# Performance work log

Measured on AMD Instinct MI355X. Metric: run time of the kernel, lower is better.

## Reference

```python
import jax, jax.numpy as jnp
import numpy as np
import math

BLOCK = 4      # block_size
N_HEADS = 8
DIM = 512
COND = 512
B = 2
HWU = 32       # h = w = u
NN = 7         # 'cross' neighbors


def _layernorm(x, w, eps=1e-5):
    mu = x.mean(-1, keepdims=True)
    var = ((x - mu) ** 2).mean(-1, keepdims=True)
    return (x - mu) * jax.lax.rsqrt(var + eps) * w


def _modulate(x, shift, scale):
    return x * (1.0 + scale) + shift


def _rotate_half(x):
    x1, x2 = jnp.split(x, 2, axis=-1)
    return jnp.concatenate([-x2, x1], axis=-1)


def _rot(x, cos, sin):
    return x * cos + _rotate_half(x) * sin


def setup_inputs() -> dict:
    key = jax.random.key(0)
    ks = jax.random.split(key, 16)
    h = w = u = HWU
    S = h * w * u
    dh = DIM // N_HEADS
    P = BLOCK ** 3
    ib = HWU // BLOCK                       # blocks per axis = 8
    nb = ib ** 3                            # 512 blocks per batch

    x = jax.random.normal(ks[0], (B, S, DIM), jnp.float32)
    c = jax.random.normal(ks[1], (B, COND), jnp.float32)

    # proper rotary tables over P block-local positions
    inv = 1.0 / (10000.0 ** (np.arange(0, dh, 2, dtype=np.float32) / dh))
    f = np.arange(P, dtype=np.float32)[:, None] * inv[None, :]
    emb = np.concatenate([f, f], axis=-1)          # [P, dh]
    cos = jnp.asarray(np.cos(emb))[None, :, None, :]
    sin = jnp.asarray(np.sin(emb))[None, :, None, :]

    # neighbor indices (cross pattern) on the block grid, mirroring get_neighbor_indices
    grid = np.stack(np.meshgrid(np.arange(B), np.arange(ib), np.arange(ib), np.arange(ib), indexing='ij'), axis=-1)
    shifts = np.array([[0, 0, 0, 0], [0, 0, -1, 0], [0, -1, 0, 0], [0, 0, 0, -1],
                       [0, 0, 1, 0], [0, 1, 0, 0], [0, 0, 0, 1]])
    nbr = grid[..., None, :] + shifts[None, None, None, None, :, :]
    nbr[..., 1:] = np.clip(nbr[..., 1:], 0, ib - 1)
    flat = (nbr[..., 0] * ib * ib * ib + nbr[..., 1] * ib * ib
            + nbr[..., 2] * ib + nbr[..., 3]).reshape(B * nb, NN)
    # every other block is 'nonzero' -> Nsel = 512
    nonzero_blocks = np.arange(0, B * nb, 2, dtype=np.int64)
    nonzero_blocks_neighbor = flat[nonzero_blocks].reshape(-1).astype(np.int64)

    s = 0.02
    params = dict(
        norm1_w=jnp.ones((DIM,), jnp.float32),
        qkv_w=s * jax.random.normal(ks[2], (3 * DIM, DIM), jnp.float32),
        out_w=s * jax.random.normal(ks[3], (DIM, DIM), jnp.float32),
        norm2_w=jnp.ones((DIM,), jnp.float32),
        mlp_w1=s * jax.random.normal(ks[4], (4 * DIM, DIM), jnp.float32),
        mlp_b1=jnp.zeros((4 * DIM,), jnp.float32),
        mlp_w2=s * jax.random.normal(ks[5], (DIM, 4 * DIM), jnp.float32),
        mlp_b2=jnp.zeros((DIM,), jnp.float32),
        adaln_w=s * jax.random.normal(ks[6], (6 * DIM, COND), jnp.float32),
        adaln_b=jnp.zeros((6 * DIM,), jnp.float32),
        kv_empty=s * jax.random.normal(ks[7], (1, P, 2 * DIM), jnp.float32),
    )
    return dict(x=x, c=c, cos_q=cos, sin_q=sin, cos_k=cos, sin_k=sin,
                nonzero_blocks=jnp.asarray(nonzero_blocks),
                nonzero_blocks_neighbor=jnp.asarray(nonzero_blocks_neighbor),
                h=h, w=w, u=u, **params)


def reference(x, c, cos_q, sin_q, cos_k, sin_k, nonzero_blocks, nonzero_blocks_neighbor,
              h, w, u, norm1_w, qkv_w, out_w, norm2_w, mlp_w1, mlp_b1, mlp_w2, mlp_b2,
              adaln_w, adaln_b, kv_empty):
    Bx, S, D = x.shape
    bs = BLOCK
    ix, iy, iz = h // bs, w // bs, u // bs
    nb = ix * iy * iz
    P = bs ** 3
    dh = D // N_HEADS
    Nsel = nonzero_blocks.shape[0]

    def transform(t):
        t = t.reshape(Bx, ix, bs, iy, bs, iz, bs, D)
        return t.transpose(0, 1, 3, 5, 2, 4, 6, 7).reshape(Bx, nb, P, D)

    def inverse_transform(t):
        t = t.reshape(Bx, ix, iy, iz, bs, bs, bs, D)
        return t.transpose(0, 1, 4, 2, 5, 3, 6, 7).reshape(Bx, S, D)

    mods = (c @ adaln_w.T + adaln_b)[:, None, :]         # [B,1,6D]
    shift_msa, scale_msa, gate_msa, shift_mlp, scale_mlp, gate_mlp = jnp.split(mods, 6, axis=-1)

    x_skip = x
    xm = _modulate(_layernorm(x, norm1_w), shift_msa, scale_msa)
    xb = transform(xm).reshape(Bx * nb, P, D)
    x_sel = xb[nonzero_blocks]                            # [Nsel,P,D]

    qkv = x_sel @ qkv_w.T                                 # [Nsel,P,3D]
    q, k, v = jnp.split(qkv, 3, axis=-1)
    k_e, v_e = jnp.split(kv_empty, 2, axis=-1)            # [1,P,D]
    k_full = jnp.broadcast_to(k_e, (Bx * nb, P, D)).at[nonzero_blocks].set(k)
    v_full = jnp.broadcast_to(v_e, (Bx * nb, P, D)).at[nonzero_blocks].set(v)
    kn = k_full[nonzero_blocks_neighbor]                  # [Nsel*NN,P,D]
    vn = v_full[nonzero_blocks_neighbor]

    qh = _rot(q.reshape(Nsel, P, N_HEADS, dh), cos_q, sin_q)
    kh = _rot(kn.reshape(Nsel * NN, P, N_HEADS, dh), cos_k, sin_k)
    kh = kh.reshape(Nsel, NN * P, N_HEADS, dh)
    vh = vn.reshape(Nsel, NN * P, N_HEADS, dh)

    scores = jnp.einsum('bqhd,bkhd->bhqk', qh, kh) / math.sqrt(dh)
    attn = jax.nn.softmax(scores, axis=-1)
    out = jnp.einsum('bhqk,bkhd->bqhd', attn, vh).reshape(Nsel, P, D)

    xz = jnp.zeros((Bx * nb, P, D), out.dtype).at[nonzero_blocks].set(out)
    x_attn = inverse_transform(xz.reshape(Bx, nb, P, D))
    x1 = x_skip + gate_msa * (x_attn @ out_w.T)

    x2 = _modulate(_layernorm(x1, norm2_w), shift_mlp, scale_mlp)
    mlp = jax.nn.gelu(x2 @ mlp_w1.T + mlp_b1, approximate=True) @ mlp_w2.T + mlp_b2
    return x1 + gate_mlp * mlp
```

## Files before the change

kernel.cpp:

```cpp
#include <hip/hip_runtime.h>
#include <cstdint>
#include <cstddef>

typedef unsigned short u16;
typedef __attribute__((ext_vector_type(8))) __bf16 bf16x8;
typedef __attribute__((ext_vector_type(4))) float f32x4;

typedef __attribute__((address_space(1))) const void GAS;
typedef __attribute__((address_space(3))) void LAS;

__device__ __forceinline__ void gld_lds16(const void* g, void* l) {
  __builtin_amdgcn_global_load_lds((GAS*)g, (LAS*)l, 16, 0, 0);
}

__device__ __forceinline__ u16 f2bf(float f) {
  union { float f; unsigned u; } x; x.f = f;
  unsigned r = x.u + 0x7FFFu + ((x.u >> 16) & 1u);
  return (u16)(r >> 16);
}
__device__ __forceinline__ float bf2f(u16 s) {
  union { unsigned u; float f; } x; x.u = ((unsigned)s) << 16;
  return x.f;
}
__device__ __forceinline__ f32x4 mfma16(bf16x8 a, bf16x8 b, f32x4 c) {
  return __builtin_amdgcn_mfma_f32_16x16x32_bf16(a, b, c, 0, 0, 0);
}


__global__ void selmap_k(const int* __restrict__ nzb, int* __restrict__ map) {
  int t = threadIdx.x;
  map[t] = -1;
  __syncthreads();
  if (t < 512) map[nzb[t]] = t;
}

__global__ __launch_bounds__(256) void castw_k(const float* __restrict__ in,
                                               u16* __restrict__ out, int n4) {
  int i = blockIdx.x * 256 + threadIdx.x;
  if (i >= n4) return;
  float4 v = ((const float4*)in)[i];
  u16 o[4] = {f2bf(v.x), f2bf(v.y), f2bf(v.z), f2bf(v.w)};
  ((uint2*)out)[i] = *(uint2*)o;
}

__global__ __launch_bounds__(256) void adaln_k(const float* __restrict__ c,
    const float* __restrict__ w, const float* __restrict__ b, float* __restrict__ mods) {
  int j = blockIdx.x * 256 + threadIdx.x;
  int bt = blockIdx.y;
  const float4* cr = (const float4*)(c + bt * 512);
  const float4* wr = (const float4*)(w + (size_t)j * 512);
  float s = 0.f;
  #pragma unroll 4
  for (int k = 0; k < 128; ++k) {
    float4 a = wr[k], q = cr[k];
    s += a.x * q.x + a.y * q.y + a.z * q.z + a.w * q.w;
  }
  mods[bt * 3072 + j] = s + b[j];
}

__global__ __launch_bounds__(256) void kvempty_k(const float* __restrict__ kve,
    const float* __restrict__ cT, const float* __restrict__ sT,
    u16* __restrict__ kempty, u16* __restrict__ vTempty) {
  int T = blockIdx.x * 256 + threadIdx.x;
  int h = T >> 12, p = (T >> 6) & 63, d = T & 63;
  float kv = kve[p * 1024 + h * 64 + d];
  float pv = kve[p * 1024 + h * 64 + (d ^ 32)];
  float cs = cT[p * 64 + d], sn = sT[p * 64 + d];
  float r = kv * cs + ((d < 32) ? -pv : pv) * sn;
  kempty[(h * 64 + p) * 64 + d] = f2bf(r);
  vTempty[(h * 64 + d) * 64 + p] = f2bf(kve[p * 1024 + 512 + h * 64 + d]);
}


__global__ __launch_bounds__(256) void ln1_k(const float* __restrict__ x,
    const float* __restrict__ nw, const float* __restrict__ mods,
    const int* __restrict__ nzb, u16* __restrict__ xm) {
  int row0 = blockIdx.x * 16 + (threadIdx.x >> 6) * 4;
  int t = threadIdx.x & 63;
  int sel = row0 >> 6, p = row0 & 63;
  int g = nzb[sel];
  int bt = g >> 9, blk = g & 511;
  int s = (blk >> 6) * 4096 + (p >> 4) * 1024 + ((blk >> 3) & 7) * 128
        + ((p >> 2) & 3) * 32 + (blk & 7) * 4 + (p & 3);
  const float* src = x + ((size_t)bt * 32768 + s) * 512;
  int d0 = t * 8;
  float v[4][8];
  #pragma unroll
  for (int rr = 0; rr < 4; ++rr) {
    float4 a = *(const float4*)(src + rr * 512 + d0);
    float4 b = *(const float4*)(src + rr * 512 + d0 + 4);
    v[rr][0] = a.x; v[rr][1] = a.y; v[rr][2] = a.z; v[rr][3] = a.w;
    v[rr][4] = b.x; v[rr][5] = b.y; v[rr][6] = b.z; v[rr][7] = b.w;
  }
  const float* mb = mods + bt * 3072;
  float wv[8], sh[8], sc[8];
  #pragma unroll
  for (int j = 0; j < 8; ++j) {
    wv[j] = nw[d0 + j]; sh[j] = mb[d0 + j]; sc[j] = mb[512 + d0 + j];
  }
  #pragma unroll
  for (int rr = 0; rr < 4; ++rr) {
    float sum = 0.f, sq = 0.f;
    #pragma unroll
    for (int j = 0; j < 8; ++j) { sum += v[rr][j]; sq += v[rr][j] * v[rr][j]; }
    #pragma unroll
    for (int m = 1; m < 64; m <<= 1) {
      sum += __shfl_xor(sum, m, 64);
      sq  += __shfl_xor(sq, m, 64);
    }
    float mean = sum * (1.f / 512.f);
    float var = sq * (1.f / 512.f) - mean * mean;
    float rstd = rsqrtf(var + 1e-5f);
    u16 o[8];
    #pragma unroll
    for (int j = 0; j < 8; ++j) {
      float xn = (v[rr][j] - mean) * rstd * wv[j];
      o[j] = f2bf(xn * (1.f + sc[j]) + sh[j]);
    }
    *(uint4*)(xm + (size_t)(row0 + rr) * 512 + d0) = *(uint4*)o;
  }
}


template <int EPI>
__global__ __launch_bounds__(256, 4) void gemm128(const u16* __restrict__ A,
    const u16* __restrict__ W, int M, int N, int K, void* __restrict__ outp,
    const float* __restrict__ bias, const u16* __restrict__ x1,
    const float* __restrict__ mods, int NB) {
  __shared__ u16 L[2][8192];
  const int nwg = gridDim.x;
  const int cpx = nwg >> 3;
  const int tile = ((int)blockIdx.x & 7) * cpx + ((int)blockIdx.x >> 3);
  const int bm = (tile / NB) * 128, bn = (tile % NB) * 128;
  const int tid = threadIdx.x;
  const int w = tid >> 6, l = tid & 63, lr = l & 15, lg = l >> 4;
  const int wr = w >> 1, wc = w & 1;

  const int s0 = tid, s1 = 256 + tid;
  const int rA0 = s0 >> 2, j0 = (s0 & 3) ^ ((s0 >> 3) & 3);
  const int rA1 = s1 >> 2, j1 = (s1 & 3) ^ ((s1 >> 3) & 3);
  const u16* gA0 = A + (size_t)(bm + rA0) * K + j0 * 8;
  const u16* gA1 = A + (size_t)(bm + rA1) * K + j1 * 8;
  const u16* gB0 = W + (size_t)(bn + rA0) * K + j0 * 8;
  const u16* gB1 = W + (size_t)(bn + rA1) * K + j1 * 8;

  f32x4 acc[4][4];
  #pragma unroll
  for (int i = 0; i < 4; ++i)
    #pragma unroll
    for (int j = 0; j < 4; ++j) acc[i][j] = (f32x4){0.f, 0.f, 0.f, 0.f};

  auto STAGE = [&](int kt, int buf) {
    u16* lb = &L[buf][0];
    gld_lds16(gA0 + (size_t)kt * 32, lb + s0 * 8);
    gld_lds16(gA1 + (size_t)kt * 32, lb + s1 * 8);
    gld_lds16(gB0 + (size_t)kt * 32, lb + 4096 + s0 * 8);
    gld_lds16(gB1 + (size_t)kt * 32, lb + 4096 + s1 * 8);
  };
  auto COMPUTE = [&](int buf) {
    const u16* base = &L[buf][0];
    bf16x8 bfr[4];
    #pragma unroll
    for (int nf = 0; nf < 4; ++nf) {
      int rB = wc * 64 + nf * 16 + lr;
      bfr[nf] = *(const bf16x8*)(base + 4096 + rB * 32 + ((lg ^ ((rB >> 1) & 3)) << 3));
    }
    __builtin_amdgcn_s_setprio(1);
    #pragma unroll
    for (int mf = 0; mf < 4; ++mf) {
      int rA = wr * 64 + mf * 16 + lr;
      bf16x8 a = *(const bf16x8*)(base + rA * 32 + ((lg ^ ((rA >> 1) & 3)) << 3));
      #pragma unroll
      for (int nf = 0; nf < 4; ++nf)
        acc[mf][nf] = mfma16(a, bfr[nf], acc[mf][nf]);
    }
    __builtin_amdgcn_s_setprio(0);
  };

  const int NT = K >> 5;
  STAGE(0, 0);
  for (int t = 0; t < NT; ++t) {
    if (t + 1 < NT) {
      STAGE(t + 1, (t + 1) & 1);
      asm volatile("s_waitcnt vmcnt(4)" ::: "memory");
    } else {
      asm volatile("s_waitcnt vmcnt(0)" ::: "memory");
    }
    __builtin_amdgcn_sched_barrier(0);
    __builtin_amdgcn_s_barrier();
    asm volatile("" ::: "memory");
    COMPUTE(t & 1);
    asm volatile("" ::: "memory");
    __builtin_amdgcn_s_barrier();
    __builtin_amdgcn_sched_barrier(0);
  }

  const int row0 = bm + wr * 64, col0 = bn + wc * 64;
  #pragma unroll
  for (int mf = 0; mf < 4; ++mf) {
    #pragma unroll
    for (int nf = 0; nf < 4; ++nf) {
      #pragma unroll
      for (int j = 0; j < 4; ++j) {
        int row = row0 + mf * 16 + lg * 4 + j;
        int col = col0 + nf * 16 + lr;
        float v = acc[mf][nf][j];
        if constexpr (EPI == 0) {
          ((u16*)outp)[(size_t)row * N + col] = f2bf(v);
        } else if constexpr (EPI == 2) {
          v += bias[col];
          float sg = 1.f / (1.f + __expf(-1.702f * v));
          ((u16*)outp)[(size_t)row * N + col] = f2bf(v * sg);
        } else {
          v += bias[col];
          int bt = row >> 15;
          float gate = mods[bt * 3072 + 2560 + col];
          ((float*)outp)[(size_t)row * 512 + col] =
              bf2f(x1[(size_t)row * 512 + col]) + gate * v;
        }
      }
    }
  }
}


__global__ __launch_bounds__(256) void ropepack_k(const u16* __restrict__ qkv,
    const float* __restrict__ cq, const float* __restrict__ sq,
    const float* __restrict__ ck, const float* __restrict__ sk,
    u16* __restrict__ qb, u16* __restrict__ kb) {
  int T = blockIdx.x * 256 + threadIdx.x;
  int row = T >> 7, oct = T & 127;
  int c0 = oct * 8;
  int sel = row >> 6, p = row & 63;
  int isk = (c0 >= 512);
  int chn = c0 & 511;
  int h = chn >> 6, d0 = chn & 63;
  int lower = (d0 < 32);
  const u16* base = qkv + (size_t)row * 1536 + (isk ? 512 : 0) + h * 64;
  u16 vm[8], vp[8];
  *(uint4*)vm = *(const uint4*)(base + d0);
  *(uint4*)vp = *(const uint4*)(base + (d0 ^ 32));
  const float* cT = (isk ? ck : cq) + p * 64 + d0;
  const float* sT = (isk ? sk : sq) + p * 64 + d0;
  float scale = isk ? 1.f : 0.125f;
  u16 o[8];
  #pragma unroll
  for (int j = 0; j < 8; ++j) {
    float a = bf2f(vm[j]), b = bf2f(vp[j]);
    float r = a * cT[j] + (lower ? -b : b) * sT[j];
    o[j] = f2bf(r * scale);
  }
  u16* dst = (isk ? kb : qb) + (((size_t)sel * 8 + h) * 64 + p) * 64 + d0;
  *(uint4*)dst = *(uint4*)o;
}


__global__ __launch_bounds__(256) void vtrans_k(const u16* __restrict__ qkv,
                                                u16* __restrict__ vT) {
  __shared__ u16 tb[64 * 65];
  int sel = blockIdx.x >> 3, h = blockIdx.x & 7;
  int tid = threadIdx.x;
  int p = tid >> 2, q16 = (tid & 3) * 16;
  const u16* src = qkv + (size_t)(sel * 64 + p) * 1536 + 1024 + h * 64 + q16;
  u16 ld[16];
  *(uint4*)&ld[0] = *(const uint4*)src;
  *(uint4*)&ld[8] = *(const uint4*)(src + 8);
  #pragma unroll
  for (int j = 0; j < 16; ++j) tb[p * 65 + q16 + j] = ld[j];
  __syncthreads();
  int d = tid >> 2, po = (tid & 3) * 16;
  u16 o[16];
  #pragma unroll
  for (int j = 0; j < 16; ++j) o[j] = tb[(po + j) * 65 + d];
  u16* dst = vT + (((size_t)sel * 8 + h) * 64 + d) * 64 + po;
  *(uint4*)dst = *(uint4*)&o[0];
  *(uint4*)(dst + 8) = *(uint4*)&o[8];
}


__global__ __launch_bounds__(256, 4) void attn_k(const u16* __restrict__ qbuf,
    const u16* __restrict__ kfull, const u16* __restrict__ vT,
    const u16* __restrict__ kempty, const u16* __restrict__ vTempty,
    const int* __restrict__ nbrs, const int* __restrict__ selmap,
    u16* __restrict__ attnout) {
  __shared__ u16 Pl[4][16][72];
  int bid = blockIdx.x;
  int swz = (bid & 7) * 512 + (bid >> 3);
  int sel = swz >> 3, h = swz & 7;
  int tid = threadIdx.x;
  int w = tid >> 6, l = tid & 63, lr = l & 15, lg = l >> 4;

  int mmv[7];
  #pragma unroll
  for (int n = 0; n < 7; ++n) mmv[n] = selmap[nbrs[sel * 7 + n]];

  const u16* qg = qbuf + (((size_t)sel * 8 + h) * 64 + w * 16) * 64;
  bf16x8 qf0 = *(const bf16x8*)(qg + lr * 64 + lg * 8);
  bf16x8 qf1 = *(const bf16x8*)(qg + lr * 64 + 32 + lg * 8);
  size_t hoff = (size_t)h * 4096;

  f32x4 o[4];
  float mrun[4], lrun[4];
  #pragma unroll
  for (int ct = 0; ct < 4; ++ct) o[ct] = (f32x4){0.f, 0.f, 0.f, 0.f};
  #pragma unroll
  for (int r = 0; r < 4; ++r) { mrun[r] = -1e30f; lrun[r] = 0.f; }

  #pragma unroll
  for (int n = 0; n < 7; ++n) {
    const u16* kp = (mmv[n] >= 0) ? kfull + (size_t)mmv[n] * 32768 + hoff
                                  : kempty + hoff;
    const u16* vp = (mmv[n] >= 0) ? vT + (size_t)mmv[n] * 32768 + hoff
                                  : vTempty + hoff;
    f32x4 s4[4];
    #pragma unroll
    for (int ct = 0; ct < 4; ++ct) {
      bf16x8 b0 = *(const bf16x8*)(kp + (ct * 16 + lr) * 64 + lg * 8);
      bf16x8 b1 = *(const bf16x8*)(kp + (ct * 16 + lr) * 64 + 32 + lg * 8);
      f32x4 z = (f32x4){0.f, 0.f, 0.f, 0.f};
      z = mfma16(qf0, b0, z);
      z = mfma16(qf1, b1, z);
      s4[ct] = z;
    }
    float rmax[4], sc[4], rs[4];
    #pragma unroll
    for (int r = 0; r < 4; ++r)
      rmax[r] = fmaxf(fmaxf(s4[0][r], s4[1][r]), fmaxf(s4[2][r], s4[3][r]));
    #pragma unroll
    for (int r = 0; r < 4; ++r) {
      #pragma unroll
      for (int ms = 1; ms < 16; ms <<= 1)
        rmax[r] = fmaxf(rmax[r], __shfl_xor(rmax[r], ms, 64));
      float mn = fmaxf(mrun[r], rmax[r]);
      sc[r] = __expf(mrun[r] - mn);
      mrun[r] = mn;
      rs[r] = 0.f;
    }
    #pragma unroll
    for (int ct = 0; ct < 4; ++ct)
      #pragma unroll
      for (int r = 0; r < 4; ++r) {
        float e = __expf(s4[ct][r] - mrun[r]);
        s4[ct][r] = e;
        rs[r] += e;
      }
    #pragma unroll
    for (int r = 0; r < 4; ++r) {
      #pragma unroll
      for (int ms = 1; ms < 16; ms <<= 1) rs[r] += __shfl_xor(rs[r], ms, 64);
      lrun[r] = lrun[r] * sc[r] + rs[r];
    }
    #pragma unroll
    for (int ct = 0; ct < 4; ++ct)
      #pragma unroll
      for (int r = 0; r < 4; ++r) o[ct][r] *= sc[r];
    #pragma unroll
    for (int ct = 0; ct < 4; ++ct)
      #pragma unroll
      for (int r = 0; r < 4; ++r)
        Pl[w][lg * 4 + r][ct * 16 + lr] = f2bf(s4[ct][r]);
    asm volatile("s_waitcnt lgkmcnt(0)" ::: "memory");
    __builtin_amdgcn_sched_barrier(0);
    bf16x8 pa0 = *(const bf16x8*)&Pl[w][lr][lg * 8];
    bf16x8 pa1 = *(const bf16x8*)&Pl[w][lr][32 + lg * 8];
    #pragma unroll
    for (int ct = 0; ct < 4; ++ct) {
      bf16x8 v0 = *(const bf16x8*)(vp + (ct * 16 + lr) * 64 + lg * 8);
      bf16x8 v1 = *(const bf16x8*)(vp + (ct * 16 + lr) * 64 + 32 + lg * 8);
      o[ct] = mfma16(pa0, v0, o[ct]);
      o[ct] = mfma16(pa1, v1, o[ct]);
    }
    __builtin_amdgcn_sched_barrier(0);
  }

  float inv[4];
  #pragma unroll
  for (int r = 0; r < 4; ++r) inv[r] = 1.f / lrun[r];
  #pragma unroll
  for (int ct = 0; ct < 4; ++ct)
    #pragma unroll
    for (int r = 0; r < 4; ++r) {
      int p = w * 16 + lg * 4 + r;
      int d = ct * 16 + lr;
      attnout[((size_t)sel * 64 + p) * 512 + h * 64 + d] = f2bf(o[ct][r] * inv[r]);
    }
}


__global__ __launch_bounds__(256) void x1ln2_k(const float* __restrict__ x,
    const u16* __restrict__ opout, const int* __restrict__ selmap,
    const float* __restrict__ mods, const float* __restrict__ nw,
    u16* __restrict__ x1, u16* __restrict__ x2) {
  int row0 = blockIdx.x * 16 + (threadIdx.x >> 6) * 4;
  int t = threadIdx.x & 63;
  int bt = row0 >> 15, s = row0 & 32767;
  int i1 = s >> 12, p1 = (s >> 10) & 3, i2 = (s >> 7) & 7,
      p2 = (s >> 5) & 3, i3 = (s >> 2) & 7, p3 = s & 3;
  int blk = (((i1 << 3) | i2) << 3) | i3;
  int m = selmap[(bt << 9) | blk];
  int p0 = (p1 << 4) | (p2 << 2) | p3;
  int d0 = t * 8;
  const float* src = x + (size_t)row0 * 512 + d0;
  float v[4][8];
  #pragma unroll
  for (int rr = 0; rr < 4; ++rr) {
    float4 a = *(const float4*)(src + rr * 512);
    float4 b = *(const float4*)(src + rr * 512 + 4);
    v[rr][0] = a.x; v[rr][1] = a.y; v[rr][2] = a.z; v[rr][3] = a.w;
    v[rr][4] = b.x; v[rr][5] = b.y; v[rr][6] = b.z; v[rr][7] = b.w;
  }
  const float* mb = mods + bt * 3072;
  float gm[8], sh2[8], sc2[8], wv[8];
  #pragma unroll
  for (int j = 0; j < 8; ++j) {
    gm[j] = mb[1024 + d0 + j]; sh2[j] = mb[1536 + d0 + j];
    sc2[j] = mb[2048 + d0 + j]; wv[j] = nw[d0 + j];
  }
  if (m >= 0) {
    const u16* op = opout + ((size_t)m * 64 + p0) * 512 + d0;
    #pragma unroll
    for (int rr = 0; rr < 4; ++rr) {
      u16 oh[8];
      *(uint4*)oh = *(const uint4*)(op + rr * 512);
      #pragma unroll
      for (int j = 0; j < 8; ++j) v[rr][j] += gm[j] * bf2f(oh[j]);
    }
  }
  #pragma unroll
  for (int rr = 0; rr < 4; ++rr) {
    u16 o1[8];
    #pragma unroll
    for (int j = 0; j < 8; ++j) o1[j] = f2bf(v[rr][j]);
    *(uint4*)(x1 + (size_t)(row0 + rr) * 512 + d0) = *(uint4*)o1;
    float sum = 0.f, sq = 0.f;
    #pragma unroll
    for (int j = 0; j < 8; ++j) { sum += v[rr][j]; sq += v[rr][j] * v[rr][j]; }
    #pragma unroll
    for (int mm = 1; mm < 64; mm <<= 1) {
      sum += __shfl_xor(sum, mm, 64);
      sq  += __shfl_xor(sq, mm, 64);
    }
    float mean = sum * (1.f / 512.f);
    float var = sq * (1.f / 512.f) - mean * mean;
    float rstd = rsqrtf(var + 1e-5f);
    u16 o[8];
    #pragma unroll
    for (int j = 0; j < 8; ++j) {
      float xn = (v[rr][j] - mean) * rstd * wv[j];
      o[j] = f2bf(xn * (1.f + sc2[j]) + sh2[j]);
    }
    *(uint4*)(x2 + (size_t)(row0 + rr) * 512 + d0) = *(uint4*)o;
  }
}


extern "C" void kernel_launch(void* const* d_in, const int* in_sizes, int n_in,
                              void* d_out, int out_size, void* d_ws, size_t ws_size,
                              hipStream_t stream) {
  const float* x    = (const float*)d_in[0];
  const float* c    = (const float*)d_in[1];
  const float* cosq = (const float*)d_in[2];
  const float* sinq = (const float*)d_in[3];
  const float* cosk = (const float*)d_in[4];
  const float* sink = (const float*)d_in[5];
  const int* nzb    = (const int*)d_in[6];
  const int* nbrs   = (const int*)d_in[7];
  const float* norm1_w = (const float*)d_in[11];
  const float* qkv_w   = (const float*)d_in[12];
  const float* out_w   = (const float*)d_in[13];
  const float* norm2_w = (const float*)d_in[14];
  const float* mlp_w1  = (const float*)d_in[15];
  const float* mlp_b1  = (const float*)d_in[16];
  const float* mlp_w2  = (const float*)d_in[17];
  const float* mlp_b2  = (const float*)d_in[18];
  const float* adaln_w = (const float*)d_in[19];
  const float* adaln_b = (const float*)d_in[20];
  const float* kv_e    = (const float*)d_in[21];
  float* outp = (float*)d_out;
  char* ws = (char*)d_ws;

  const size_t MB = 1024ull * 1024ull;
  u16*   qkvb    = (u16*)(ws + 0);
  u16*   opout   = (u16*)(ws + 0);
  u16*   hidden  = (u16*)(ws + 0);
  u16*   xm      = (u16*)(ws + 96 * MB);
  u16*   attnout = (u16*)(ws + 96 * MB);
  u16*   qb      = (u16*)(ws + 128 * MB);
  u16*   kf      = (u16*)(ws + 160 * MB);
  u16*   vT      = (u16*)(ws + 192 * MB);
  u16*   x1      = (u16*)(ws + 256 * MB);
  u16*   x2      = (u16*)(ws + 320 * MB);
  char*  S0      = ws + 384 * MB;
  float* mods    = (float*)(S0);
  int*   selmap  = (int*)(S0 + 0x8000);
  u16*   kempty  = (u16*)(S0 + 0x10000);
  u16*   vTempty = (u16*)(S0 + 0x20000);
  u16*   qkvw_bf = (u16*)(S0 + 0x30000);
  u16*   outw_bf = qkvw_bf + (size_t)1536 * 512;
  u16*   w1_bf   = outw_bf + (size_t)512 * 512;
  u16*   w2_bf   = w1_bf + (size_t)2048 * 512;

  selmap_k<<<1, 1024, 0, stream>>>(nzb, selmap);
  adaln_k<<<dim3(12, 2), 256, 0, stream>>>(c, adaln_w, adaln_b, mods);
  castw_k<<<768, 256, 0, stream>>>(qkv_w, qkvw_bf, 1536 * 512 / 4);
  castw_k<<<256, 256, 0, stream>>>(out_w, outw_bf, 512 * 512 / 4);
  castw_k<<<1024, 256, 0, stream>>>(mlp_w1, w1_bf, 2048 * 512 / 4);
  castw_k<<<1024, 256, 0, stream>>>(mlp_w2, w2_bf, 512 * 2048 / 4);
  kvempty_k<<<128, 256, 0, stream>>>(kv_e, cosk, sink, kempty, vTempty);

  ln1_k<<<2048, 256, 0, stream>>>(x, norm1_w, mods, nzb, xm);

  gemm128<0><<<3072, 256, 0, stream>>>(xm, qkvw_bf, 32768, 1536, 512, qkvb,
                                       nullptr, nullptr, nullptr, 12);
  ropepack_k<<<16384, 256, 0, stream>>>(qkvb, cosq, sinq, cosk, sink, qb, kf);
  vtrans_k<<<4096, 256, 0, stream>>>(qkvb, vT);

  attn_k<<<4096, 256, 0, stream>>>(qb, kf, vT, kempty, vTempty, nbrs, selmap, attnout);

  gemm128<0><<<1024, 256, 0, stream>>>(attnout, outw_bf, 32768, 512, 512, opout,
                                       nullptr, nullptr, nullptr, 4);

  x1ln2_k<<<4096, 256, 0, stream>>>(x, opout, selmap, mods, norm2_w, x1, x2);

  gemm128<2><<<8192, 256, 0, stream>>>(x2, w1_bf, 65536, 2048, 512, hidden,
                                       mlp_b1, nullptr, nullptr, 16);
  gemm128<3><<<2048, 256, 0, stream>>>(hidden, w2_bf, 65536, 512, 2048, outp,
                                       mlp_b2, x1, mods, 4);
}
```

Measured before the change: 855.4 us.

## Double-buffer K tiles into LDS via async global-to-LDS loads in attention

The attention kernel now stages each neighbor's K tile into a swizzled, double-buffered LDS array using global_load_lds. The next neighbor's tile is prefetched while the current one is computed. This is meant to hide global load latency and share K loads across the four waves instead of each wave loading K directly. It adds two workgroup barriers per iteration and 16KB of LDS, and raises the occupancy hint in launch bounds from 4 to 6.

```diff
diff --git a/kernel.cpp b/kernel.cpp
--- a/kernel.cpp
+++ b/kernel.cpp
@@ -278,11 +278,12 @@
 }
 
 
-__global__ __launch_bounds__(256, 4) void attn_k(const u16* __restrict__ qbuf,
+__global__ __launch_bounds__(256, 6) void attn_k(const u16* __restrict__ qbuf,
     const u16* __restrict__ kfull, const u16* __restrict__ vT,
     const u16* __restrict__ kempty, const u16* __restrict__ vTempty,
     const int* __restrict__ nbrs, const int* __restrict__ selmap,
     u16* __restrict__ attnout) {
+  __shared__ u16 KB[2][4096];
   __shared__ u16 Pl[4][16][72];
   int bid = blockIdx.x;
   int swz = (bid & 7) * 512 + (bid >> 3);
@@ -297,7 +298,17 @@
   const u16* qg = qbuf + (((size_t)sel * 8 + h) * 64 + w * 16) * 64;
   bf16x8 qf0 = *(const bf16x8*)(qg + lr * 64 + lg * 8);
   bf16x8 qf1 = *(const bf16x8*)(qg + lr * 64 + 32 + lg * 8);
+
+  int srow = tid >> 3;
+  int soff = srow * 64 + (((tid & 7) ^ (srow & 7)) << 3);
   size_t hoff = (size_t)h * 4096;
+
+  {
+    const u16* kp = (mmv[0] >= 0) ? kfull + (size_t)mmv[0] * 32768 + hoff
+                                  : kempty + hoff;
+    gld_lds16(kp + soff, &KB[0][w * 512]);
+    gld_lds16(kp + soff + 2048, &KB[0][2048 + w * 512]);
+  }
 
   f32x4 o[4];
   float mrun[4], lrun[4];
@@ -308,15 +319,29 @@
 
   #pragma unroll
   for (int n = 0; n < 7; ++n) {
-    const u16* kp = (mmv[n] >= 0) ? kfull + (size_t)mmv[n] * 32768 + hoff
-                                  : kempty + hoff;
+    if (n < 6) {
+      const u16* kp = (mmv[n + 1] >= 0) ? kfull + (size_t)mmv[n + 1] * 32768 + hoff
+                                        : kempty + hoff;
+      int b = (n + 1) & 1;
+      gld_lds16(kp + soff, &KB[b][w * 512]);
+      gld_lds16(kp + soff + 2048, &KB[b][2048 + w * 512]);
+      asm volatile("s_waitcnt vmcnt(2)" ::: "memory");
+    } else {
+      asm volatile("s_waitcnt vmcnt(0)" ::: "memory");
+    }
+    __builtin_amdgcn_s_barrier();
+    __builtin_amdgcn_sched_barrier(0);
+
+    const u16* kl = &KB[n & 1][0];
     const u16* vp = (mmv[n] >= 0) ? vT + (size_t)mmv[n] * 32768 + hoff
                                   : vTempty + hoff;
     f32x4 s4[4];
+    int xr = lr & 7;
     #pragma unroll
     for (int ct = 0; ct < 4; ++ct) {
-      bf16x8 b0 = *(const bf16x8*)(kp + (ct * 16 + lr) * 64 + lg * 8);
-      bf16x8 b1 = *(const bf16x8*)(kp + (ct * 16 + lr) * 64 + 32 + lg * 8);
+      int row = ct * 16 + lr;
+      bf16x8 b0 = *(const bf16x8*)(kl + row * 64 + ((lg ^ xr) << 3));
+      bf16x8 b1 = *(const bf16x8*)(kl + row * 64 + (((lg + 4) ^ xr) << 3));
       f32x4 z = (f32x4){0.f, 0.f, 0.f, 0.f};
       z = mfma16(qf0, b0, z);
       z = mfma16(qf1, b1, z);
@@ -370,6 +395,8 @@
       o[ct] = mfma16(pa0, v0, o[ct]);
       o[ct] = mfma16(pa1, v1, o[ct]);
     }
+    asm volatile("" ::: "memory");
+    __builtin_amdgcn_s_barrier();
     __builtin_amdgcn_sched_barrier(0);
   }
 
```

Measured after the change: 831.9 us. 1.03x faster.
